# Kernel tuning notes

Measured on AMD Instinct MI355X. Metric: run time of the kernel, lower is better.

The kernel has to match this reference:

```python
import jax, jax.numpy as jnp
import numpy as np

B = 16384
S = 7
CELL = 1.0 / 7.0   # CELL_SILE
LC = 5.0           # lambda_coord
LN = 0.5           # lambda_noobj


def setup_inputs() -> dict:
    key = jax.random.key(0)
    k1, k2, k3 = jax.random.split(key, 3)
    predictions = jax.random.normal(k1, (B, S, S, 30), dtype=jnp.float32)
    targets = jax.random.uniform(k2, (B, S, S, 30), dtype=jnp.float32)
    # channel 4 is the objectness flag; code requires it to be exactly 0 or 1
    conf = (jax.random.uniform(k3, (B, S, S)) < 0.25).astype(jnp.float32)
    targets = targets.at[..., 4].set(conf)
    return {"predictions": predictions, "targets": targets}


def _box_corners(xy, wh):
    # Faithful to the original in-place bug: x2y2 uses the ALREADY-UPDATED x1y1
    xy1 = xy * CELL - wh * 0.5
    xy2 = xy1 * CELL + wh * 0.5
    return xy1, xy2


def _loss_terms(predictions, targets):
    p = predictions.reshape(-1, 30)   # [N, 30], N = B*S*S
    t = targets.reshape(-1, 30)
    obj = (t[:, 4] == 1.0).astype(p.dtype)
    noobj = (t[:, 4] == 0.0).astype(p.dtype)

    # no-object confidence loss on cols 4 and 9
    noobj_loss = LN * jnp.sum(noobj * (jnp.square(p[:, 4] - t[:, 4]) + jnp.square(p[:, 9] - t[:, 9])))

    # two predicted boxes per cell: cols 0:4 and 5:9 ; wh are sqrt-encoded -> square
    pb = jnp.stack([p[:, 0:4], p[:, 5:9]], axis=1)        # [N, 2, 4]
    pxy1, pxy2 = _box_corners(pb[..., 0:2], jnp.square(pb[..., 2:4]))  # [N,2,2]
    txy1, txy2 = _box_corners(t[:, None, 0:2], jnp.square(t[:, None, 2:4]))  # [N,1,2]

    # torchvision.ops.box_iou math (no clamp on areas, clamp(0) on intersection)
    lt = jnp.maximum(pxy1, txy1)
    rb = jnp.minimum(pxy2, txy2)
    inter = jnp.prod(jnp.clip(rb - lt, 0.0, None), axis=-1)   # [N, 2]
    area_p = jnp.prod(pxy2 - pxy1, axis=-1)                   # [N, 2]
    area_t = jnp.prod(txy2 - txy1, axis=-1)                   # [N, 1]
    iou = inter / (area_p + area_t - inter)                   # [N, 2]

    idx = jnp.argmax(iou, axis=1)                             # responsible box in {0,1}

    cols = idx[:, None] * 5 + jnp.arange(4)[None, :]          # [N, 4]
    cp = jnp.take_along_axis(p, cols, axis=1)
    ct = jnp.take_along_axis(t, cols, axis=1)
    center_loss = LC * jnp.sum(obj * jnp.sum(jnp.square(cp[:, 0:2] - ct[:, 0:2]), axis=1))
    wh_loss = LC * jnp.sum(obj * jnp.sum(jnp.square(cp[:, 2:4] - ct[:, 2:4]), axis=1))

    ccol = (idx * 5 + 4)[:, None]
    conf_loss = LC * jnp.sum(obj * jnp.square(jnp.take_along_axis(p, ccol, axis=1) - jnp.take_along_axis(t, ccol, axis=1))[:, 0])

    kcol = (jnp.argmax(t[:, 10:30], axis=1) + 10)[:, None]
    cls_loss = LC * jnp.sum(obj * jnp.square(jnp.take_along_axis(p, kcol, axis=1) - jnp.take_along_axis(t, kcol, axis=1))[:, 0])

    total = noobj_loss + center_loss + wh_loss + conf_loss + cls_loss
    return cls_loss, conf_loss, center_loss + wh_loss, total


def reference(predictions, targets):
    return _loss_terms(predictions, targets)
```

## Files before the change

kernel.cpp:

```cpp
#include <hip/hip_runtime.h>


constexpr int   BS   = 256;
constexpr int   NC   = 16384 * 7 * 7;
constexpr int   NB   = NC / BS;
constexpr float CELL = 1.0f / 7.0f;
constexpr float LC   = 5.0f;
constexpr float LN   = 0.5f;

__launch_bounds__(BS, 5)
__global__ void yolo_partial(const float* __restrict__ P, const float* __restrict__ T,
                             float4* __restrict__ ws)
{
    __shared__ float sT[BS * 30];
    __shared__ float red[4][BS / 64];

    const int tid  = threadIdx.x;
    const size_t base = (size_t)blockIdx.x * (BS * 30);

    const float* prow = P + base + (size_t)tid * 30;
    float pv[10];
    #pragma unroll
    for (int j = 0; j < 5; ++j) {
        float2 v = reinterpret_cast<const float2*>(prow)[j];
        pv[2 * j] = v.x; pv[2 * j + 1] = v.y;
    }

    const float4* gT4 = reinterpret_cast<const float4*>(T + base);
    float4* sT4 = reinterpret_cast<float4*>(sT);
    constexpr int NV4 = BS * 30 / 4;
    #pragma unroll
    for (int k = 0; k < (NV4 + BS - 1) / BS; ++k) {
        int idx = k * BS + tid;
        if (idx < NV4) sT4[idx] = gT4[idx];
    }
    __syncthreads();

    const float* tt = sT + tid * 30;
    float tv[30];
    #pragma unroll
    for (int j = 0; j < 15; ++j) {
        float2 v = reinterpret_cast<const float2*>(tt)[j];
        tv[2 * j] = v.x; tv[2 * j + 1] = v.y;
    }

    int kc = 10;
    float best = tv[10];
    #pragma unroll
    for (int k = 11; k < 30; ++k) {
        if (tv[k] > best) { best = tv[k]; kc = k; }
    }
    float pk = prow[kc];

    const float t4 = tv[4];
    const float obj   = (t4 == 1.0f) ? 1.0f : 0.0f;
    const float noobj = (t4 == 0.0f) ? 1.0f : 0.0f;

    float d4 = pv[4] - t4;
    float d9 = pv[9] - tv[9];
    float noobj_v = noobj * (d4 * d4 + d9 * d9);

    float tw2 = tv[2] * tv[2], th2 = tv[3] * tv[3];
    float tx1 = tv[0] * CELL - 0.5f * tw2;
    float tx2 = tx1 * CELL + 0.5f * tw2;
    float ty1 = tv[1] * CELL - 0.5f * th2;
    float ty2 = ty1 * CELL + 0.5f * th2;
    float area_t = (tx2 - tx1) * (ty2 - ty1);

    float iou0, iou1;
    #pragma unroll
    for (int b = 0; b < 2; ++b) {
        float bx = pv[5 * b + 0], by = pv[5 * b + 1];
        float bw2 = pv[5 * b + 2] * pv[5 * b + 2];
        float bh2 = pv[5 * b + 3] * pv[5 * b + 3];
        float px1 = bx * CELL - 0.5f * bw2;
        float px2 = px1 * CELL + 0.5f * bw2;
        float py1 = by * CELL - 0.5f * bh2;
        float py2 = py1 * CELL + 0.5f * bh2;
        float ltx = fmaxf(px1, tx1), lty = fmaxf(py1, ty1);
        float rbx = fminf(px2, tx2), rby = fminf(py2, ty2);
        float inter = fmaxf(rbx - ltx, 0.0f) * fmaxf(rby - lty, 0.0f);
        float area_p = (px2 - px1) * (py2 - py1);
        float iou = inter / (area_p + area_t - inter);
        if (b == 0) iou0 = iou; else iou1 = iou;
    }
    const bool b1 = (iou1 > iou0);

    float cpx = b1 ? pv[5] : pv[0], ctx = b1 ? tv[5] : tv[0];
    float cpy = b1 ? pv[6] : pv[1], cty = b1 ? tv[6] : tv[1];
    float cpw = b1 ? pv[7] : pv[2], ctw = b1 ? tv[7] : tv[2];
    float cph = b1 ? pv[8] : pv[3], cth = b1 ? tv[8] : tv[3];
    float cpc = b1 ? pv[9] : pv[4], ctc = b1 ? tv[9] : tv[4];

    float dx = cpx - ctx, dy = cpy - cty;
    float dw = cpw - ctw, dh = cph - cth;
    float cw_v = obj * (dx * dx + dy * dy + dw * dw + dh * dh);
    float dc = cpc - ctc;
    float conf_v = obj * dc * dc;

    float dk = pk - best;
    float cls_v = obj * dk * dk;

    float vals[4] = { cls_v, conf_v, cw_v, noobj_v };
    #pragma unroll
    for (int c = 0; c < 4; ++c) {
        float v = vals[c];
        #pragma unroll
        for (int off = 32; off > 0; off >>= 1)
            v += __shfl_down(v, off, 64);
        if ((tid & 63) == 0) red[c][tid >> 6] = v;
    }
    __syncthreads();
    if (tid == 0) {
        float4 s;
        s.x = red[0][0] + red[0][1] + red[0][2] + red[0][3];
        s.y = red[1][0] + red[1][1] + red[1][2] + red[1][3];
        s.z = red[2][0] + red[2][1] + red[2][2] + red[2][3];
        s.w = red[3][0] + red[3][1] + red[3][2] + red[3][3];
        ws[blockIdx.x] = s;
    }
}

__launch_bounds__(256, 1)
__global__ void yolo_reduce(const float4* __restrict__ ws, float* __restrict__ out)
{
    __shared__ float red[4][4];
    const int tid = threadIdx.x;

    float s0 = 0.f, s1 = 0.f, s2 = 0.f, s3 = 0.f;
    for (int b = tid; b < NB; b += 256) {
        float4 v = ws[b];
        s0 += v.x; s1 += v.y; s2 += v.z; s3 += v.w;
    }
    float vals[4] = { s0, s1, s2, s3 };
    #pragma unroll
    for (int c = 0; c < 4; ++c) {
        float v = vals[c];
        #pragma unroll
        for (int off = 32; off > 0; off >>= 1)
            v += __shfl_down(v, off, 64);
        if ((tid & 63) == 0) red[c][tid >> 6] = v;
    }
    __syncthreads();
    if (tid == 0) {
        float t0 = red[0][0] + red[0][1] + red[0][2] + red[0][3];
        float t1 = red[1][0] + red[1][1] + red[1][2] + red[1][3];
        float t2 = red[2][0] + red[2][1] + red[2][2] + red[2][3];
        float t3 = red[3][0] + red[3][1] + red[3][2] + red[3][3];
        out[0] = LC * t0;
        out[1] = LC * t1;
        out[2] = LC * t2;
        out[3] = LN * t3 + LC * (t0 + t1 + t2);
    }
}

extern "C" void kernel_launch(void* const* d_in, const int* in_sizes, int n_in,
                              void* d_out, int out_size, void* d_ws, size_t ws_size,
                              hipStream_t stream) {
    const float* P = (const float*)d_in[0];
    const float* T = (const float*)d_in[1];
    float* out = (float*)d_out;
    float4* ws = (float4*)d_ws;

    yolo_partial<<<NB, BS, 0, stream>>>(P, T, ws);
    yolo_reduce<<<1, 256, 0, stream>>>(ws, out);
}
```

Before: 209.7 us.

## Use persistent grid with register-prefetched next tile of predictions and targets

Changes the kernel from one block per 256-cell tile to a persistent grid of 1280 blocks that loop over tiles. Each block prefetches the next tile's predictions into registers and stages its targets into shared memory while computing on the current tile. Per-block partial sums accumulate across tiles, so the reduce kernel reads fewer partials. The cost is extra syncthreads per iteration and higher register pressure. Global loads issued before the compute are held up by the barriers, so the overlap may be limited.

```diff
diff --git a/kernel.cpp b/kernel.cpp
--- a/kernel.cpp
+++ b/kernel.cpp
@@ -4,9 +4,29 @@
 constexpr int   BS   = 256;
 constexpr int   NC   = 16384 * 7 * 7;
 constexpr int   NB   = NC / BS;
+constexpr int   NBLK = 1280;
 constexpr float CELL = 1.0f / 7.0f;
 constexpr float LC   = 5.0f;
 constexpr float LN   = 0.5f;
+
+__device__ __forceinline__ void load_p10(float* pv, const float* prow) {
+    #pragma unroll
+    for (int j = 0; j < 5; ++j) {
+        float2 v = reinterpret_cast<const float2*>(prow)[j];
+        pv[2 * j] = v.x; pv[2 * j + 1] = v.y;
+    }
+}
+
+__device__ __forceinline__ void stage_T(float* sT, const float* Tbase, int tid) {
+    const float4* g4 = reinterpret_cast<const float4*>(Tbase);
+    float4* s4 = reinterpret_cast<float4*>(sT);
+    constexpr int NV4 = BS * 30 / 4;
+    #pragma unroll
+    for (int k = 0; k < (NV4 + BS - 1) / BS; ++k) {
+        int idx = k * BS + tid;
+        if (idx < NV4) s4[idx] = g4[idx];
+    }
+}
 
 __launch_bounds__(BS, 5)
 __global__ void yolo_partial(const float* __restrict__ P, const float* __restrict__ T,
@@ -15,93 +35,112 @@
     __shared__ float sT[BS * 30];
     __shared__ float red[4][BS / 64];
 
-    const int tid  = threadIdx.x;
-    const size_t base = (size_t)blockIdx.x * (BS * 30);
-
-    const float* prow = P + base + (size_t)tid * 30;
+    const int tid = threadIdx.x;
+
+    float a_cls = 0.f, a_conf = 0.f, a_cw = 0.f, a_noobj = 0.f;
+
+    int tile = blockIdx.x;
+    size_t base = (size_t)tile * (BS * 30);
     float pv[10];
-    #pragma unroll
-    for (int j = 0; j < 5; ++j) {
-        float2 v = reinterpret_cast<const float2*>(prow)[j];
-        pv[2 * j] = v.x; pv[2 * j + 1] = v.y;
-    }
-
-    const float4* gT4 = reinterpret_cast<const float4*>(T + base);
-    float4* sT4 = reinterpret_cast<float4*>(sT);
-    constexpr int NV4 = BS * 30 / 4;
-    #pragma unroll
-    for (int k = 0; k < (NV4 + BS - 1) / BS; ++k) {
-        int idx = k * BS + tid;
-        if (idx < NV4) sT4[idx] = gT4[idx];
-    }
-    __syncthreads();
-
-    const float* tt = sT + tid * 30;
+    load_p10(pv, P + base + (size_t)tid * 30);
+    stage_T(sT, T + base, tid);
+    __syncthreads();
+
     float tv[30];
-    #pragma unroll
-    for (int j = 0; j < 15; ++j) {
-        float2 v = reinterpret_cast<const float2*>(tt)[j];
-        tv[2 * j] = v.x; tv[2 * j + 1] = v.y;
-    }
-
-    int kc = 10;
-    float best = tv[10];
-    #pragma unroll
-    for (int k = 11; k < 30; ++k) {
-        if (tv[k] > best) { best = tv[k]; kc = k; }
-    }
-    float pk = prow[kc];
-
-    const float t4 = tv[4];
-    const float obj   = (t4 == 1.0f) ? 1.0f : 0.0f;
-    const float noobj = (t4 == 0.0f) ? 1.0f : 0.0f;
-
-    float d4 = pv[4] - t4;
-    float d9 = pv[9] - tv[9];
-    float noobj_v = noobj * (d4 * d4 + d9 * d9);
-
-    float tw2 = tv[2] * tv[2], th2 = tv[3] * tv[3];
-    float tx1 = tv[0] * CELL - 0.5f * tw2;
-    float tx2 = tx1 * CELL + 0.5f * tw2;
-    float ty1 = tv[1] * CELL - 0.5f * th2;
-    float ty2 = ty1 * CELL + 0.5f * th2;
-    float area_t = (tx2 - tx1) * (ty2 - ty1);
-
-    float iou0, iou1;
-    #pragma unroll
-    for (int b = 0; b < 2; ++b) {
-        float bx = pv[5 * b + 0], by = pv[5 * b + 1];
-        float bw2 = pv[5 * b + 2] * pv[5 * b + 2];
-        float bh2 = pv[5 * b + 3] * pv[5 * b + 3];
-        float px1 = bx * CELL - 0.5f * bw2;
-        float px2 = px1 * CELL + 0.5f * bw2;
-        float py1 = by * CELL - 0.5f * bh2;
-        float py2 = py1 * CELL + 0.5f * bh2;
-        float ltx = fmaxf(px1, tx1), lty = fmaxf(py1, ty1);
-        float rbx = fminf(px2, tx2), rby = fminf(py2, ty2);
-        float inter = fmaxf(rbx - ltx, 0.0f) * fmaxf(rby - lty, 0.0f);
-        float area_p = (px2 - px1) * (py2 - py1);
-        float iou = inter / (area_p + area_t - inter);
-        if (b == 0) iou0 = iou; else iou1 = iou;
-    }
-    const bool b1 = (iou1 > iou0);
-
-    float cpx = b1 ? pv[5] : pv[0], ctx = b1 ? tv[5] : tv[0];
-    float cpy = b1 ? pv[6] : pv[1], cty = b1 ? tv[6] : tv[1];
-    float cpw = b1 ? pv[7] : pv[2], ctw = b1 ? tv[7] : tv[2];
-    float cph = b1 ? pv[8] : pv[3], cth = b1 ? tv[8] : tv[3];
-    float cpc = b1 ? pv[9] : pv[4], ctc = b1 ? tv[9] : tv[4];
-
-    float dx = cpx - ctx, dy = cpy - cty;
-    float dw = cpw - ctw, dh = cph - cth;
-    float cw_v = obj * (dx * dx + dy * dy + dw * dw + dh * dh);
-    float dc = cpc - ctc;
-    float conf_v = obj * dc * dc;
-
-    float dk = pk - best;
-    float cls_v = obj * dk * dk;
-
-    float vals[4] = { cls_v, conf_v, cw_v, noobj_v };
+    {
+        const float* tt = sT + tid * 30;
+        #pragma unroll
+        for (int j = 0; j < 15; ++j) {
+            float2 v = reinterpret_cast<const float2*>(tt)[j];
+            tv[2 * j] = v.x; tv[2 * j + 1] = v.y;
+        }
+    }
+    __syncthreads();
+
+    while (true) {
+        const int next = tile + NBLK;
+        const bool has_next = next < NB;
+        float pvn[10];
+        if (has_next) {
+            size_t nbase = (size_t)next * (BS * 30);
+            load_p10(pvn, P + nbase + (size_t)tid * 30);
+            stage_T(sT, T + nbase, tid);
+        }
+
+        int kc = 10;
+        float best = tv[10];
+        #pragma unroll
+        for (int k = 11; k < 30; ++k) {
+            if (tv[k] > best) { best = tv[k]; kc = k; }
+        }
+        float pk = P[base + (size_t)tid * 30 + kc];
+
+        const float t4 = tv[4];
+        const float obj   = (t4 == 1.0f) ? 1.0f : 0.0f;
+        const float noobj = (t4 == 0.0f) ? 1.0f : 0.0f;
+
+        float d4 = pv[4] - t4;
+        float d9 = pv[9] - tv[9];
+        a_noobj += noobj * (d4 * d4 + d9 * d9);
+
+        float tw2 = tv[2] * tv[2], th2 = tv[3] * tv[3];
+        float tx1 = tv[0] * CELL - 0.5f * tw2;
+        float tx2 = tx1 * CELL + 0.5f * tw2;
+        float ty1 = tv[1] * CELL - 0.5f * th2;
+        float ty2 = ty1 * CELL + 0.5f * th2;
+        float area_t = (tx2 - tx1) * (ty2 - ty1);
+
+        float iou0, iou1;
+        #pragma unroll
+        for (int b = 0; b < 2; ++b) {
+            float bw2 = pv[5 * b + 2] * pv[5 * b + 2];
+            float bh2 = pv[5 * b + 3] * pv[5 * b + 3];
+            float px1 = pv[5 * b + 0] * CELL - 0.5f * bw2;
+            float px2 = px1 * CELL + 0.5f * bw2;
+            float py1 = pv[5 * b + 1] * CELL - 0.5f * bh2;
+            float py2 = py1 * CELL + 0.5f * bh2;
+            float ltx = fmaxf(px1, tx1), lty = fmaxf(py1, ty1);
+            float rbx = fminf(px2, tx2), rby = fminf(py2, ty2);
+            float inter = fmaxf(rbx - ltx, 0.0f) * fmaxf(rby - lty, 0.0f);
+            float area_p = (px2 - px1) * (py2 - py1);
+            float iou = inter / (area_p + area_t - inter);
+            if (b == 0) iou0 = iou; else iou1 = iou;
+        }
+        const bool b1 = (iou1 > iou0);
+
+        float cpx = b1 ? pv[5] : pv[0], ctx = b1 ? tv[5] : tv[0];
+        float cpy = b1 ? pv[6] : pv[1], cty = b1 ? tv[6] : tv[1];
+        float cpw = b1 ? pv[7] : pv[2], ctw = b1 ? tv[7] : tv[2];
+        float cph = b1 ? pv[8] : pv[3], cth = b1 ? tv[8] : tv[3];
+        float cpc = b1 ? pv[9] : pv[4], ctc = b1 ? tv[9] : tv[4];
+
+        float dx = cpx - ctx, dy = cpy - cty;
+        float dw = cpw - ctw, dh = cph - cth;
+        a_cw   += obj * (dx * dx + dy * dy + dw * dw + dh * dh);
+        float dc = cpc - ctc;
+        a_conf += obj * dc * dc;
+        float dk = pk - best;
+        a_cls  += obj * dk * dk;
+
+        if (!has_next) break;
+
+        __syncthreads();
+        {
+            const float* tt = sT + tid * 30;
+            #pragma unroll
+            for (int j = 0; j < 15; ++j) {
+                float2 v = reinterpret_cast<const float2*>(tt)[j];
+                tv[2 * j] = v.x; tv[2 * j + 1] = v.y;
+            }
+        }
+        __syncthreads();
+        #pragma unroll
+        for (int j = 0; j < 10; ++j) pv[j] = pvn[j];
+        tile = next;
+        base = (size_t)tile * (BS * 30);
+    }
+
+    float vals[4] = { a_cls, a_conf, a_cw, a_noobj };
     #pragma unroll
     for (int c = 0; c < 4; ++c) {
         float v = vals[c];
@@ -128,7 +167,7 @@
     const int tid = threadIdx.x;
 
     float s0 = 0.f, s1 = 0.f, s2 = 0.f, s3 = 0.f;
-    for (int b = tid; b < NB; b += 256) {
+    for (int b = tid; b < NBLK; b += 256) {
         float4 v = ws[b];
         s0 += v.x; s1 += v.y; s2 += v.z; s3 += v.w;
     }
@@ -162,6 +201,6 @@
     float* out = (float*)d_out;
     float4* ws = (float4*)d_ws;
 
-    yolo_partial<<<NB, BS, 0, stream>>>(P, T, ws);
+    yolo_partial<<<NBLK, BS, 0, stream>>>(P, T, ws);
     yolo_reduce<<<1, 256, 0, stream>>>(ws, out);
 }
```

Measured after the change: 212.4 us. About the same (+1.3%).

## Switch to persistent single-wave blocks with grid-stride tiles and staged P loads

Applied to the files above, without the earlier changes.

Replaces one 256-thread block per 256 cells with a fixed grid of 2560 single-wavefront blocks. Each block loops over 64-cell tiles, staging both predictions and targets through LDS with coalesced float4 loads, and keeps per-lane accumulators. This removes the uncoalesced strided float2 loads of predictions and the cross-wave LDS reduction, and shrinks the partial workspace the final reduce reads. The cost is that each tile is loaded and then processed serially with two barriers per tile, so a wave gets little overlap of memory and compute. Only 64-thread blocks may also limit memory-level parallelism.

```diff
diff --git a/kernel.cpp b/kernel.cpp
--- a/kernel.cpp
+++ b/kernel.cpp
@@ -1,152 +1,149 @@
 #include <hip/hip_runtime.h>
 
 
-constexpr int   BS   = 256;
+constexpr int   WSZ  = 64;
 constexpr int   NC   = 16384 * 7 * 7;
-constexpr int   NB   = NC / BS;
+constexpr int   NT   = NC / WSZ;
+constexpr int   GRID = 2560;
 constexpr float CELL = 1.0f / 7.0f;
 constexpr float LC   = 5.0f;
 constexpr float LN   = 0.5f;
 
-__launch_bounds__(BS, 5)
+__launch_bounds__(WSZ, 2)
 __global__ void yolo_partial(const float* __restrict__ P, const float* __restrict__ T,
                              float4* __restrict__ ws)
 {
-    __shared__ float sT[BS * 30];
-    __shared__ float red[4][BS / 64];
+    __shared__ float sP[WSZ * 30];
+    __shared__ float sT[WSZ * 30];
 
-    const int tid  = threadIdx.x;
-    const size_t base = (size_t)blockIdx.x * (BS * 30);
+    const int lane = threadIdx.x;
+    float a_cls = 0.f, a_conf = 0.f, a_cw = 0.f, a_noobj = 0.f;
 
-    const float* prow = P + base + (size_t)tid * 30;
-    float pv[10];
-    #pragma unroll
-    for (int j = 0; j < 5; ++j) {
-        float2 v = reinterpret_cast<const float2*>(prow)[j];
-        pv[2 * j] = v.x; pv[2 * j + 1] = v.y;
+    for (int tile = blockIdx.x; tile < NT; tile += GRID) {
+        const size_t base = (size_t)tile * (WSZ * 30);
+
+        const float4* gP = reinterpret_cast<const float4*>(P + base);
+        const float4* gT = reinterpret_cast<const float4*>(T + base);
+        float4* s4P = reinterpret_cast<float4*>(sP);
+        float4* s4T = reinterpret_cast<float4*>(sT);
+        constexpr int NV4 = WSZ * 30 / 4;
+        #pragma unroll
+        for (int k = 0; k < 8; ++k) {
+            int idx = k * WSZ + lane;
+            if (idx < NV4) { s4P[idx] = gP[idx]; s4T[idx] = gT[idx]; }
+        }
+        __syncthreads();
+
+        const float* tt = sT + lane * 30;
+        const float* tp = sP + lane * 30;
+        float tv[30];
+        #pragma unroll
+        for (int j = 0; j < 15; ++j) {
+            float2 v = reinterpret_cast<const float2*>(tt)[j];
+            tv[2 * j] = v.x; tv[2 * j + 1] = v.y;
+        }
+        float pv[10];
+        #pragma unroll
+        for (int j = 0; j < 5; ++j) {
+            float2 v = reinterpret_cast<const float2*>(tp)[j];
+            pv[2 * j] = v.x; pv[2 * j + 1] = v.y;
+        }
+
+        int kc = 10;
+        float best = tv[10];
+        #pragma unroll
+        for (int k = 11; k < 30; ++k) {
+            if (tv[k] > best) { best = tv[k]; kc = k; }
+        }
+        float pk = tp[kc];
+
+        const float t4 = tv[4];
+        const float obj   = (t4 == 1.0f) ? 1.0f : 0.0f;
+        const float noobj = (t4 == 0.0f) ? 1.0f : 0.0f;
+
+        float d4 = pv[4] - t4;
+        float d9 = pv[9] - tv[9];
+        a_noobj += noobj * (d4 * d4 + d9 * d9);
+
+        float tw2 = tv[2] * tv[2], th2 = tv[3] * tv[3];
+        float tx1 = tv[0] * CELL - 0.5f * tw2;
+        float tx2 = tx1 * CELL + 0.5f * tw2;
+        float ty1 = tv[1] * CELL - 0.5f * th2;
+        float ty2 = ty1 * CELL + 0.5f * th2;
+        float area_t = (tx2 - tx1) * (ty2 - ty1);
+
+        float iou0, iou1;
+        #pragma unroll
+        for (int b = 0; b < 2; ++b) {
+            float bw2 = pv[5 * b + 2] * pv[5 * b + 2];
+            float bh2 = pv[5 * b + 3] * pv[5 * b + 3];
+            float px1 = pv[5 * b + 0] * CELL - 0.5f * bw2;
+            float px2 = px1 * CELL + 0.5f * bw2;
+            float py1 = pv[5 * b + 1] * CELL - 0.5f * bh2;
+            float py2 = py1 * CELL + 0.5f * bh2;
+            float ltx = fmaxf(px1, tx1), lty = fmaxf(py1, ty1);
+            float rbx = fminf(px2, tx2), rby = fminf(py2, ty2);
+            float inter = fmaxf(rbx - ltx, 0.0f) * fmaxf(rby - lty, 0.0f);
+            float area_p = (px2 - px1) * (py2 - py1);
+            float iou = inter / (area_p + area_t - inter);
+            if (b == 0) iou0 = iou; else iou1 = iou;
+        }
+        const bool b1 = (iou1 > iou0);
+
+        float cpx = b1 ? pv[5] : pv[0], ctx = b1 ? tv[5] : tv[0];
+        float cpy = b1 ? pv[6] : pv[1], cty = b1 ? tv[6] : tv[1];
+        float cpw = b1 ? pv[7] : pv[2], ctw = b1 ? tv[7] : tv[2];
+        float cph = b1 ? pv[8] : pv[3], cth = b1 ? tv[8] : tv[3];
+        float cpc = b1 ? pv[9] : pv[4], ctc = b1 ? tv[9] : tv[4];
+
+        float dx = cpx - ctx, dy = cpy - cty;
+        float dw = cpw - ctw, dh = cph - cth;
+        a_cw   += obj * (dx * dx + dy * dy + dw * dw + dh * dh);
+        float dc = cpc - ctc;
+        a_conf += obj * dc * dc;
+        float dk = pk - best;
+        a_cls  += obj * dk * dk;
+
+        __syncthreads();
     }
 
-    const float4* gT4 = reinterpret_cast<const float4*>(T + base);
-    float4* sT4 = reinterpret_cast<float4*>(sT);
-    constexpr int NV4 = BS * 30 / 4;
-    #pragma unroll
-    for (int k = 0; k < (NV4 + BS - 1) / BS; ++k) {
-        int idx = k * BS + tid;
-        if (idx < NV4) sT4[idx] = gT4[idx];
-    }
-    __syncthreads();
-
-    const float* tt = sT + tid * 30;
-    float tv[30];
-    #pragma unroll
-    for (int j = 0; j < 15; ++j) {
-        float2 v = reinterpret_cast<const float2*>(tt)[j];
-        tv[2 * j] = v.x; tv[2 * j + 1] = v.y;
-    }
-
-    int kc = 10;
-    float best = tv[10];
-    #pragma unroll
-    for (int k = 11; k < 30; ++k) {
-        if (tv[k] > best) { best = tv[k]; kc = k; }
-    }
-    float pk = prow[kc];
-
-    const float t4 = tv[4];
-    const float obj   = (t4 == 1.0f) ? 1.0f : 0.0f;
-    const float noobj = (t4 == 0.0f) ? 1.0f : 0.0f;
-
-    float d4 = pv[4] - t4;
-    float d9 = pv[9] - tv[9];
-    float noobj_v = noobj * (d4 * d4 + d9 * d9);
-
-    float tw2 = tv[2] * tv[2], th2 = tv[3] * tv[3];
-    float tx1 = tv[0] * CELL - 0.5f * tw2;
-    float tx2 = tx1 * CELL + 0.5f * tw2;
-    float ty1 = tv[1] * CELL - 0.5f * th2;
-    float ty2 = ty1 * CELL + 0.5f * th2;
-    float area_t = (tx2 - tx1) * (ty2 - ty1);
-
-    float iou0, iou1;
-    #pragma unroll
-    for (int b = 0; b < 2; ++b) {
-        float bx = pv[5 * b + 0], by = pv[5 * b + 1];
-        float bw2 = pv[5 * b + 2] * pv[5 * b + 2];
-        float bh2 = pv[5 * b + 3] * pv[5 * b + 3];
-        float px1 = bx * CELL - 0.5f * bw2;
-        float px2 = px1 * CELL + 0.5f * bw2;
-        float py1 = by * CELL - 0.5f * bh2;
-        float py2 = py1 * CELL + 0.5f * bh2;
-        float ltx = fmaxf(px1, tx1), lty = fmaxf(py1, ty1);
-        float rbx = fminf(px2, tx2), rby = fminf(py2, ty2);
-        float inter = fmaxf(rbx - ltx, 0.0f) * fmaxf(rby - lty, 0.0f);
-        float area_p = (px2 - px1) * (py2 - py1);
-        float iou = inter / (area_p + area_t - inter);
-        if (b == 0) iou0 = iou; else iou1 = iou;
-    }
-    const bool b1 = (iou1 > iou0);
-
-    float cpx = b1 ? pv[5] : pv[0], ctx = b1 ? tv[5] : tv[0];
-    float cpy = b1 ? pv[6] : pv[1], cty = b1 ? tv[6] : tv[1];
-    float cpw = b1 ? pv[7] : pv[2], ctw = b1 ? tv[7] : tv[2];
-    float cph = b1 ? pv[8] : pv[3], cth = b1 ? tv[8] : tv[3];
-    float cpc = b1 ? pv[9] : pv[4], ctc = b1 ? tv[9] : tv[4];
-
-    float dx = cpx - ctx, dy = cpy - cty;
-    float dw = cpw - ctw, dh = cph - cth;
-    float cw_v = obj * (dx * dx + dy * dy + dw * dw + dh * dh);
-    float dc = cpc - ctc;
-    float conf_v = obj * dc * dc;
-
-    float dk = pk - best;
-    float cls_v = obj * dk * dk;
-
-    float vals[4] = { cls_v, conf_v, cw_v, noobj_v };
+    float vals[4] = { a_cls, a_conf, a_cw, a_noobj };
     #pragma unroll
     for (int c = 0; c < 4; ++c) {
-        float v = vals[c];
         #pragma unroll
         for (int off = 32; off > 0; off >>= 1)
-            v += __shfl_down(v, off, 64);
-        if ((tid & 63) == 0) red[c][tid >> 6] = v;
+            vals[c] += __shfl_down(vals[c], off, 64);
     }
-    __syncthreads();
-    if (tid == 0) {
-        float4 s;
-        s.x = red[0][0] + red[0][1] + red[0][2] + red[0][3];
-        s.y = red[1][0] + red[1][1] + red[1][2] + red[1][3];
-        s.z = red[2][0] + red[2][1] + red[2][2] + red[2][3];
-        s.w = red[3][0] + red[3][1] + red[3][2] + red[3][3];
-        ws[blockIdx.x] = s;
-    }
+    if (lane == 0)
+        ws[blockIdx.x] = make_float4(vals[0], vals[1], vals[2], vals[3]);
 }
 
-__launch_bounds__(256, 1)
+__launch_bounds__(1024, 1)
 __global__ void yolo_reduce(const float4* __restrict__ ws, float* __restrict__ out)
 {
-    __shared__ float red[4][4];
+    __shared__ float red[4][16];
     const int tid = threadIdx.x;
 
     float s0 = 0.f, s1 = 0.f, s2 = 0.f, s3 = 0.f;
-    for (int b = tid; b < NB; b += 256) {
+    for (int b = tid; b < GRID; b += 1024) {
         float4 v = ws[b];
         s0 += v.x; s1 += v.y; s2 += v.z; s3 += v.w;
     }
     float vals[4] = { s0, s1, s2, s3 };
     #pragma unroll
     for (int c = 0; c < 4; ++c) {
-        float v = vals[c];
         #pragma unroll
         for (int off = 32; off > 0; off >>= 1)
-            v += __shfl_down(v, off, 64);
-        if ((tid & 63) == 0) red[c][tid >> 6] = v;
+            vals[c] += __shfl_down(vals[c], off, 64);
+        if ((tid & 63) == 0) red[c][tid >> 6] = vals[c];
     }
     __syncthreads();
     if (tid == 0) {
-        float t0 = red[0][0] + red[0][1] + red[0][2] + red[0][3];
-        float t1 = red[1][0] + red[1][1] + red[1][2] + red[1][3];
-        float t2 = red[2][0] + red[2][1] + red[2][2] + red[2][3];
-        float t3 = red[3][0] + red[3][1] + red[3][2] + red[3][3];
+        float t0 = 0.f, t1 = 0.f, t2 = 0.f, t3 = 0.f;
+        #pragma unroll
+        for (int w = 0; w < 16; ++w) {
+            t0 += red[0][w]; t1 += red[1][w]; t2 += red[2][w]; t3 += red[3][w];
+        }
         out[0] = LC * t0;
         out[1] = LC * t1;
         out[2] = LC * t2;
@@ -162,6 +159,6 @@
     float* out = (float*)d_out;
     float4* ws = (float4*)d_ws;
 
-    yolo_partial<<<NB, BS, 0, stream>>>(P, T, ws);
-    yolo_reduce<<<1, 256, 0, stream>>>(ws, out);
+    yolo_partial<<<GRID, WSZ, 0, stream>>>(P, T, ws);
+    yolo_reduce<<<1, 1024, 0, stream>>>(ws, out);
 }
```

Result: no change. 207.5 us (-1.0%).
